# Kernel tuning notes

Measured on AMD Instinct MI355X. Metric: run time of the kernel, lower is better.

## Reference

```python
import jax, jax.numpy as jnp
import numpy as np

# NF4 codebook (bitsandbytes NormalFloat4 quantiles)
NF4_TABLE = jnp.array([
    -1.0, -0.6961928009986877, -0.5250730514526367, -0.39491748809814453,
    -0.28444138169288635, -0.18477343022823334, -0.09105003625154495, 0.0,
    0.07958029955625534, 0.16093020141124725, 0.24611230194568634,
    0.33791524171829224, 0.44070982933044434, 0.5626170039176941,
    0.7229568362236023, 1.0], dtype=jnp.float32)

BLOCK = 64  # bitsandbytes default quantization blocksize


def setup_inputs() -> dict:
    key = jax.random.key(0)
    ks = jax.random.split(key, 6)
    in_f, out_f, rank, n_tok = 4096, 4096, 16, 8192
    x = jax.random.normal(ks[0], (n_tok, in_f), dtype=jnp.float32)
    q_codes = jax.random.randint(ks[1], (out_f, in_f), 0, 16, dtype=jnp.int32)
    absmax = jax.random.uniform(ks[2], (out_f, in_f // BLOCK), dtype=jnp.float32) * 0.1 + 1e-3
    bias = jax.random.normal(ks[3], (out_f,), dtype=jnp.float32) * 0.02
    # kaiming-uniform-ish init for lora_down; lora_up nonzero for a meaningful test
    lora_down_w = jax.random.normal(ks[4], (rank, in_f), dtype=jnp.float32) * (1.0 / np.sqrt(in_f))
    lora_up_w = jax.random.normal(ks[5], (out_f, rank), dtype=jnp.float32) * 0.02
    alpha = jnp.array(16.0, dtype=jnp.float32)
    return {"x": x, "absmax": absmax, "bias": bias, "lora_down_w": lora_down_w,
            "lora_up_w": lora_up_w, "alpha": alpha, "q_codes": q_codes}


def reference(x, absmax, bias, lora_down_w, lora_up_w, alpha, q_codes):
    rank = lora_down_w.shape[0]
    # dequantize NF4 base weight: code lookup * per-block absmax scale
    w = NF4_TABLE[q_codes] * jnp.repeat(absmax, BLOCK, axis=1)  # [out, in]
    base = x @ w.T + bias                                       # [n_tok, out]
    # LoRA path: down [rank,in], up [out,rank], scaled by alpha/rank
    lora = (x @ lora_down_w.T) @ lora_up_w.T                    # [n_tok, out]
    return base + lora * (alpha / rank)
```

## Files before the change

kernel.cpp:

```cpp
#include <hip/hip_runtime.h>

#define IN_F 4096
#define OUT_F 4096
#define RANK 16
#define NTOK 8192
#define KP 4160
#define BK 64
#define NT (KP / BK)
#define BM 256
#define BN 256

typedef __bf16 bf16x8 __attribute__((ext_vector_type(8)));
typedef float f32x4 __attribute__((ext_vector_type(4)));

__device__ __forceinline__ unsigned short f2bf(float f) {
  unsigned int u = __float_as_uint(f);
  u += 0x7fffu + ((u >> 16) & 1u);
  return (unsigned short)(u >> 16);
}

__device__ __forceinline__ void async_ld16(const void* g, void* l) {
  __builtin_amdgcn_global_load_lds(
      (const __attribute__((address_space(1))) unsigned int*)g,
      (__attribute__((address_space(3))) unsigned int*)l, 16, 0, 0);
}

__device__ const float NF4_TAB[16] = {
    -1.0f, -0.6961928009986877f, -0.5250730514526367f, -0.39491748809814453f,
    -0.28444138169288635f, -0.18477343022823334f, -0.09105003625154495f, 0.0f,
    0.07958029955625534f, 0.16093020141124725f, 0.24611230194568634f,
    0.33791524171829224f, 0.44070982933044434f, 0.5626170039176941f,
    0.7229568362236023f, 1.0f};

__global__ __launch_bounds__(256) void k_prep_a(
    const float* __restrict__ x, const float* __restrict__ ldw,
    unsigned short* __restrict__ Ap) {
  const int tid = threadIdx.x;
  const int lane = tid & 63;
  const int w = tid >> 6;
  const int m0 = blockIdx.x * 4;

  float acc[4][4];
#pragma unroll
  for (int i = 0; i < 4; ++i)
#pragma unroll
    for (int rl = 0; rl < 4; ++rl) acc[i][rl] = 0.f;

  for (int c = 0; c < 16; ++c) {
    const int k0 = (c * 64 + lane) * 4;
    float4 xv[4];
#pragma unroll
    for (int i = 0; i < 4; ++i) {
      xv[i] = *(const float4*)&x[(size_t)(m0 + i) * IN_F + k0];
      if (w == 0) {
        ushort4 s;
        s.x = f2bf(xv[i].x); s.y = f2bf(xv[i].y);
        s.z = f2bf(xv[i].z); s.w = f2bf(xv[i].w);
        *(ushort4*)&Ap[(size_t)(m0 + i) * KP + k0] = s;
      }
    }
#pragma unroll
    for (int rl = 0; rl < 4; ++rl) {
      float4 lv = *(const float4*)&ldw[(size_t)(w * 4 + rl) * IN_F + k0];
#pragma unroll
      for (int i = 0; i < 4; ++i)
        acc[i][rl] += xv[i].x * lv.x + xv[i].y * lv.y + xv[i].z * lv.z +
                      xv[i].w * lv.w;
    }
  }
#pragma unroll
  for (int i = 0; i < 4; ++i)
#pragma unroll
    for (int rl = 0; rl < 4; ++rl) {
      float v = acc[i][rl];
#pragma unroll
      for (int m = 1; m < 64; m <<= 1) v += __shfl_xor(v, m, 64);
      acc[i][rl] = v;
    }
  __shared__ float red[4][16];
  if (lane == 0) {
#pragma unroll
    for (int i = 0; i < 4; ++i)
#pragma unroll
      for (int rl = 0; rl < 4; ++rl) red[i][w * 4 + rl] = acc[i][rl];
  }
  __syncthreads();
  if (tid < 64) {
    Ap[(size_t)(m0 + (tid >> 4)) * KP + IN_F + (tid & 15)] =
        f2bf(red[tid >> 4][tid & 15]);
  } else {
    const int t2 = tid - 64;
    if (t2 < 192)
      Ap[(size_t)(m0 + t2 / 48) * KP + IN_F + 16 + (t2 % 48)] = 0;
  }
}

__global__ __launch_bounds__(256) void k_prep_b(
    const int* __restrict__ q, const float* __restrict__ amax,
    const float* __restrict__ luw, const float* __restrict__ alpha,
    unsigned short* __restrict__ Bp) {
  __shared__ float tab[16];
  const int tid = threadIdx.x;
  const int n = blockIdx.x;
  if (tid < 16) tab[tid] = NF4_TAB[tid];
  __syncthreads();
#pragma unroll
  for (int c = 0; c < 4; ++c) {
    const int k0 = (tid + 256 * c) * 4;
    int4 qv = *(const int4*)&q[(size_t)n * IN_F + k0];
    float am = amax[n * (IN_F / 64) + (k0 >> 6)];
    ushort4 s;
    s.x = f2bf(tab[qv.x] * am);
    s.y = f2bf(tab[qv.y] * am);
    s.z = f2bf(tab[qv.z] * am);
    s.w = f2bf(tab[qv.w] * am);
    *(ushort4*)&Bp[(size_t)n * KP + k0] = s;
  }
  if (tid < RANK) {
    float sc = alpha[0] * (1.0f / RANK);
    Bp[(size_t)n * KP + IN_F + tid] = f2bf(luw[n * RANK + tid] * sc);
  } else if (tid < 64) {
    Bp[(size_t)n * KP + IN_F + tid] = 0;
  }
}

__global__ __launch_bounds__(512, 1) void k_gemm(
    const unsigned short* __restrict__ Ap, const unsigned short* __restrict__ Bp,
    const float* __restrict__ bias, float* __restrict__ out) {
  __shared__ unsigned short lds[65536];
  const int tid = threadIdx.x;
  const int lane = tid & 63;
  const int w = tid >> 6;
  const int wr = w >> 2;
  const int wc = w & 3;

  const int nwg = gridDim.x * gridDim.y;
  const int flat = blockIdx.y * gridDim.x + blockIdx.x;
  const int cpx = nwg >> 3;
  const int swz = (flat & 7) * cpx + (flat >> 3);
  const int m0 = (swz / (OUT_F / BN)) * BM;
  const int n0 = (swz % (OUT_F / BN)) * BN;

  const int srow = lane >> 3;
  const int scol = (((lane & 7) ^ srow) << 3);
  const unsigned short* gA = Ap + (size_t)(m0 + (w << 4) + srow) * KP + scol;
  const unsigned short* gB = Bp + (size_t)(n0 + (w << 4) + srow) * KP + scol;
  unsigned short* const ldsw = lds + (w << 10);

  const int rdoff = ((lane & 15) << 6) + (((lane >> 4) ^ (lane & 7)) << 3);

#define STAGE2(tt, ht, cond)                                                   \
  if (cond) {                                                                  \
    const unsigned short* s_ =                                                 \
        ((ht) < 2 ? gA + (size_t)((ht) << 7) * KP                              \
                  : gB + (size_t)(((ht)-2) << 7) * KP) + (size_t)(tt)*BK;      \
    unsigned short* d_ = ldsw + ((((tt)&1) << 15) + ((ht) << 13));             \
    async_ld16(s_, d_);                                                        \
    async_ld16(s_ + (size_t)8 * KP, d_ + 512);                                 \
  }

#define LDA(bsel, mh, f, kc)                                                   \
  (*(const bf16x8*)&lds[((bsel) << 15) + (wr << 13) +                          \
                        (((mh)*64 + (f)*16) << 6) + (((kc) << 5) ^ rdoff)])
#define LDB(bsel, nh, g, kc)                                                   \
  (*(const bf16x8*)&lds[((bsel) << 15) + ((2 + (wc >> 1)) << 13) +             \
                        ((((wc & 1) * 64) + (nh)*32 + (g)*16) << 6) +          \
                        (((kc) << 5) ^ rdoff)])

#define MFMA(a, b, c) __builtin_amdgcn_mfma_f32_16x16x32_bf16((a), (b), (c), 0, 0, 0)

  STAGE2(0, 0, true) STAGE2(0, 1, true) STAGE2(0, 2, true) STAGE2(0, 3, true)
  STAGE2(1, 0, true) STAGE2(1, 1, true)
  asm volatile("s_waitcnt vmcnt(4)" ::: "memory");
  __builtin_amdgcn_s_barrier();

  f32x4 acc[8][4] = {};
  bf16x8 a0[4][2], a1[4][2], bq[2][2];

#pragma unroll 2
  for (int t = 0; t < NT; ++t) {
    const int bsel = t & 1;
#pragma unroll
    for (int f = 0; f < 4; ++f) {
      a0[f][0] = LDA(bsel, 0, f, 0);
      a0[f][1] = LDA(bsel, 0, f, 1);
    }
#pragma unroll
    for (int g = 0; g < 2; ++g) {
      bq[g][0] = LDB(bsel, 0, g, 0);
      bq[g][1] = LDB(bsel, 0, g, 1);
    }
    STAGE2(t + 1, 2, t + 1 < NT)
    __builtin_amdgcn_s_barrier();
    asm volatile("s_waitcnt lgkmcnt(0)" ::: "memory");
    __builtin_amdgcn_sched_barrier(0);
    __builtin_amdgcn_s_setprio(1);
#pragma unroll
    for (int f = 0; f < 4; ++f)
#pragma unroll
      for (int g = 0; g < 2; ++g) {
        acc[f][g] = MFMA(a0[f][0], bq[g][0], acc[f][g]);
        acc[f][g] = MFMA(a0[f][1], bq[g][1], acc[f][g]);
      }
    __builtin_amdgcn_s_setprio(0);
    __builtin_amdgcn_s_barrier();
#pragma unroll
    for (int f = 0; f < 4; ++f) {
      a1[f][0] = LDA(bsel, 1, f, 0);
      a1[f][1] = LDA(bsel, 1, f, 1);
    }
    STAGE2(t + 1, 3, t + 1 < NT)
    __builtin_amdgcn_s_barrier();
    asm volatile("s_waitcnt lgkmcnt(0)" ::: "memory");
    __builtin_amdgcn_sched_barrier(0);
    __builtin_amdgcn_s_setprio(1);
#pragma unroll
    for (int f = 0; f < 4; ++f)
#pragma unroll
      for (int g = 0; g < 2; ++g) {
        acc[4 + f][g] = MFMA(a1[f][0], bq[g][0], acc[4 + f][g]);
        acc[4 + f][g] = MFMA(a1[f][1], bq[g][1], acc[4 + f][g]);
      }
    __builtin_amdgcn_s_setprio(0);
    __builtin_amdgcn_s_barrier();
#pragma unroll
    for (int g = 0; g < 2; ++g) {
      bq[g][0] = LDB(bsel, 1, g, 0);
      bq[g][1] = LDB(bsel, 1, g, 1);
    }
    STAGE2(t + 2, 0, t + 2 < NT)
    __builtin_amdgcn_s_barrier();
    asm volatile("s_waitcnt lgkmcnt(0)" ::: "memory");
    __builtin_amdgcn_sched_barrier(0);
    __builtin_amdgcn_s_setprio(1);
#pragma unroll
    for (int f = 0; f < 4; ++f)
#pragma unroll
      for (int g = 0; g < 2; ++g) {
        acc[4 + f][2 + g] = MFMA(a1[f][0], bq[g][0], acc[4 + f][2 + g]);
        acc[4 + f][2 + g] = MFMA(a1[f][1], bq[g][1], acc[4 + f][2 + g]);
      }
    __builtin_amdgcn_s_setprio(0);
    __builtin_amdgcn_s_barrier();
    STAGE2(t + 2, 1, t + 2 < NT)
    __builtin_amdgcn_s_barrier();
    asm volatile("s_waitcnt lgkmcnt(0)" ::: "memory");
    __builtin_amdgcn_sched_barrier(0);
    __builtin_amdgcn_s_setprio(1);
#pragma unroll
    for (int f = 0; f < 4; ++f)
#pragma unroll
      for (int g = 0; g < 2; ++g) {
        acc[f][2 + g] = MFMA(a0[f][0], bq[g][0], acc[f][2 + g]);
        acc[f][2 + g] = MFMA(a0[f][1], bq[g][1], acc[f][2 + g]);
      }
    __builtin_amdgcn_s_setprio(0);
    if (t < NT - 2) {
      asm volatile("s_waitcnt vmcnt(4)" ::: "memory");
    } else if (t == NT - 2) {
      asm volatile("s_waitcnt vmcnt(0)" ::: "memory");
    }
    __builtin_amdgcn_s_barrier();
    __builtin_amdgcn_sched_barrier(0);
  }

  const int colL = lane & 15;
  const int rowG = lane >> 4;
#pragma unroll
  for (int nj = 0; nj < 4; ++nj) {
    const int n = n0 + wc * 64 + nj * 16 + colL;
    const float bv = bias[n];
#pragma unroll
    for (int mi = 0; mi < 8; ++mi) {
      const int mb = m0 + wr * 128 + mi * 16 + rowG * 4;
#pragma unroll
      for (int e = 0; e < 4; ++e)
        out[(size_t)(mb + e) * OUT_F + n] = acc[mi][nj][e] + bv;
    }
  }
#undef STAGE2
#undef LDA
#undef LDB
#undef MFMA
}

extern "C" void kernel_launch(void* const* d_in, const int* in_sizes, int n_in,
                              void* d_out, int out_size, void* d_ws, size_t ws_size,
                              hipStream_t stream) {
  (void)in_sizes; (void)n_in; (void)out_size; (void)ws_size;
  const float* x     = (const float*)d_in[0];
  const float* amax  = (const float*)d_in[1];
  const float* bias  = (const float*)d_in[2];
  const float* ldw   = (const float*)d_in[3];
  const float* luw   = (const float*)d_in[4];
  const float* alpha = (const float*)d_in[5];
  const int*   q     = (const int*)d_in[6];
  float* out = (float*)d_out;

  unsigned short* Ap = (unsigned short*)d_ws;
  unsigned short* Bp = Ap + (size_t)NTOK * KP;

  k_prep_a<<<NTOK / 4, 256, 0, stream>>>(x, ldw, Ap);
  k_prep_b<<<OUT_F, 256, 0, stream>>>(q, amax, luw, alpha, Bp);
  k_gemm<<<dim3(OUT_F / BN, NTOK / BM), 512, 0, stream>>>(Ap, Bp, bias, out);
}
```

Baseline: 351.3 us.

## Switch main GEMM to 32x32x16 bf16 MFMA with reworked LDS fragment loads

Replaces the 16x16x32 MFMA tiling with 32x32x16 MFMA instructions, restructuring the per-wave fragment loads from swizzled LDS and the accumulator layout (f32x16 tiles), plus a matching epilogue. The larger MFMA cuts the number of LDS fragment reads per flop and the instruction count. It also drops one lgkmcnt wait before the last MFMA group, since that group reuses already-loaded registers. Separately, the prep kernel now spreads the bf16 conversion stores across four waves instead of one.

```diff
diff --git a/kernel.cpp b/kernel.cpp
--- a/kernel.cpp
+++ b/kernel.cpp
@@ -12,6 +12,7 @@
 
 typedef __bf16 bf16x8 __attribute__((ext_vector_type(8)));
 typedef float f32x4 __attribute__((ext_vector_type(4)));
+typedef float f32x16 __attribute__((ext_vector_type(16)));
 
 __device__ __forceinline__ unsigned short f2bf(float f) {
   unsigned int u = __float_as_uint(f);
@@ -52,7 +53,7 @@
 #pragma unroll
     for (int i = 0; i < 4; ++i) {
       xv[i] = *(const float4*)&x[(size_t)(m0 + i) * IN_F + k0];
-      if (w == 0) {
+      if (w == i) {
         ushort4 s;
         s.x = f2bf(xv[i].x); s.y = f2bf(xv[i].y);
         s.z = f2bf(xv[i].z); s.w = f2bf(xv[i].w);
@@ -147,7 +148,9 @@
   const unsigned short* gB = Bp + (size_t)(n0 + (w << 4) + srow) * KP + scol;
   unsigned short* const ldsw = lds + (w << 10);
 
-  const int rdoff = ((lane & 15) << 6) + (((lane >> 4) ^ (lane & 7)) << 3);
+  const int rowA = (lane & 31) << 6;
+  const int hi = lane >> 5;
+  const int sw = lane & 7;
 
 #define STAGE2(tt, ht, cond)                                                   \
   if (cond) {                                                                  \
@@ -159,36 +162,32 @@
     async_ld16(s_ + (size_t)8 * KP, d_ + 512);                                 \
   }
 
-#define LDA(bsel, mh, f, kc)                                                   \
-  (*(const bf16x8*)&lds[((bsel) << 15) + (wr << 13) +                          \
-                        (((mh)*64 + (f)*16) << 6) + (((kc) << 5) ^ rdoff)])
-#define LDB(bsel, nh, g, kc)                                                   \
+#define LDA32(bsel, tm, s)                                                     \
+  (*(const bf16x8*)&lds[((bsel) << 15) + (wr << 13) + ((tm) << 11) + rowA +    \
+                        (((((s) << 1) | hi) ^ sw) << 3)])
+#define LDB32(bsel, tn, s)                                                     \
   (*(const bf16x8*)&lds[((bsel) << 15) + ((2 + (wc >> 1)) << 13) +             \
-                        ((((wc & 1) * 64) + (nh)*32 + (g)*16) << 6) +          \
-                        (((kc) << 5) ^ rdoff)])
-
-#define MFMA(a, b, c) __builtin_amdgcn_mfma_f32_16x16x32_bf16((a), (b), (c), 0, 0, 0)
+                        ((wc & 1) << 12) + ((tn) << 11) + rowA +               \
+                        (((((s) << 1) | hi) ^ sw) << 3)])
+
+#define MFMA32(a, b, c) __builtin_amdgcn_mfma_f32_32x32x16_bf16((a), (b), (c), 0, 0, 0)
 
   STAGE2(0, 0, true) STAGE2(0, 1, true) STAGE2(0, 2, true) STAGE2(0, 3, true)
   STAGE2(1, 0, true) STAGE2(1, 1, true)
   asm volatile("s_waitcnt vmcnt(4)" ::: "memory");
   __builtin_amdgcn_s_barrier();
 
-  f32x4 acc[8][4] = {};
-  bf16x8 a0[4][2], a1[4][2], bq[2][2];
+  f32x16 acc[4][2] = {};
+  bf16x8 a01[2][4], a23[2][4], bq[4];
 
 #pragma unroll 2
   for (int t = 0; t < NT; ++t) {
     const int bsel = t & 1;
 #pragma unroll
-    for (int f = 0; f < 4; ++f) {
-      a0[f][0] = LDA(bsel, 0, f, 0);
-      a0[f][1] = LDA(bsel, 0, f, 1);
-    }
-#pragma unroll
-    for (int g = 0; g < 2; ++g) {
-      bq[g][0] = LDB(bsel, 0, g, 0);
-      bq[g][1] = LDB(bsel, 0, g, 1);
+    for (int s = 0; s < 4; ++s) {
+      a01[0][s] = LDA32(bsel, 0, s);
+      a01[1][s] = LDA32(bsel, 1, s);
+      bq[s] = LDB32(bsel, 0, s);
     }
     STAGE2(t + 1, 2, t + 1 < NT)
     __builtin_amdgcn_s_barrier();
@@ -196,18 +195,16 @@
     __builtin_amdgcn_sched_barrier(0);
     __builtin_amdgcn_s_setprio(1);
 #pragma unroll
-    for (int f = 0; f < 4; ++f)
-#pragma unroll
-      for (int g = 0; g < 2; ++g) {
-        acc[f][g] = MFMA(a0[f][0], bq[g][0], acc[f][g]);
-        acc[f][g] = MFMA(a0[f][1], bq[g][1], acc[f][g]);
-      }
-    __builtin_amdgcn_s_setprio(0);
-    __builtin_amdgcn_s_barrier();
-#pragma unroll
-    for (int f = 0; f < 4; ++f) {
-      a1[f][0] = LDA(bsel, 1, f, 0);
-      a1[f][1] = LDA(bsel, 1, f, 1);
+    for (int s = 0; s < 4; ++s) {
+      acc[0][0] = MFMA32(a01[0][s], bq[s], acc[0][0]);
+      acc[1][0] = MFMA32(a01[1][s], bq[s], acc[1][0]);
+    }
+    __builtin_amdgcn_s_setprio(0);
+    __builtin_amdgcn_s_barrier();
+#pragma unroll
+    for (int s = 0; s < 4; ++s) {
+      a23[0][s] = LDA32(bsel, 2, s);
+      a23[1][s] = LDA32(bsel, 3, s);
     }
     STAGE2(t + 1, 3, t + 1 < NT)
     __builtin_amdgcn_s_barrier();
@@ -215,45 +212,35 @@
     __builtin_amdgcn_sched_barrier(0);
     __builtin_amdgcn_s_setprio(1);
 #pragma unroll
-    for (int f = 0; f < 4; ++f)
-#pragma unroll
-      for (int g = 0; g < 2; ++g) {
-        acc[4 + f][g] = MFMA(a1[f][0], bq[g][0], acc[4 + f][g]);
-        acc[4 + f][g] = MFMA(a1[f][1], bq[g][1], acc[4 + f][g]);
-      }
-    __builtin_amdgcn_s_setprio(0);
-    __builtin_amdgcn_s_barrier();
-#pragma unroll
-    for (int g = 0; g < 2; ++g) {
-      bq[g][0] = LDB(bsel, 1, g, 0);
-      bq[g][1] = LDB(bsel, 1, g, 1);
-    }
+    for (int s = 0; s < 4; ++s) {
+      acc[2][0] = MFMA32(a23[0][s], bq[s], acc[2][0]);
+      acc[3][0] = MFMA32(a23[1][s], bq[s], acc[3][0]);
+    }
+    __builtin_amdgcn_s_setprio(0);
+    __builtin_amdgcn_s_barrier();
+#pragma unroll
+    for (int s = 0; s < 4; ++s) bq[s] = LDB32(bsel, 1, s);
     STAGE2(t + 2, 0, t + 2 < NT)
     __builtin_amdgcn_s_barrier();
     asm volatile("s_waitcnt lgkmcnt(0)" ::: "memory");
     __builtin_amdgcn_sched_barrier(0);
     __builtin_amdgcn_s_setprio(1);
 #pragma unroll
-    for (int f = 0; f < 4; ++f)
-#pragma unroll
-      for (int g = 0; g < 2; ++g) {
-        acc[4 + f][2 + g] = MFMA(a1[f][0], bq[g][0], acc[4 + f][2 + g]);
-        acc[4 + f][2 + g] = MFMA(a1[f][1], bq[g][1], acc[4 + f][2 + g]);
-      }
+    for (int s = 0; s < 4; ++s) {
+      acc[2][1] = MFMA32(a23[0][s], bq[s], acc[2][1]);
+      acc[3][1] = MFMA32(a23[1][s], bq[s], acc[3][1]);
+    }
     __builtin_amdgcn_s_setprio(0);
     __builtin_amdgcn_s_barrier();
     STAGE2(t + 2, 1, t + 2 < NT)
     __builtin_amdgcn_s_barrier();
-    asm volatile("s_waitcnt lgkmcnt(0)" ::: "memory");
-    __builtin_amdgcn_sched_barrier(0);
-    __builtin_amdgcn_s_setprio(1);
-#pragma unroll
-    for (int f = 0; f < 4; ++f)
-#pragma unroll
-      for (int g = 0; g < 2; ++g) {
-        acc[f][2 + g] = MFMA(a0[f][0], bq[g][0], acc[f][2 + g]);
-        acc[f][2 + g] = MFMA(a0[f][1], bq[g][1], acc[f][2 + g]);
-      }
+    __builtin_amdgcn_sched_barrier(0);
+    __builtin_amdgcn_s_setprio(1);
+#pragma unroll
+    for (int s = 0; s < 4; ++s) {
+      acc[0][1] = MFMA32(a01[0][s], bq[s], acc[0][1]);
+      acc[1][1] = MFMA32(a01[1][s], bq[s], acc[1][1]);
+    }
     __builtin_amdgcn_s_setprio(0);
     if (t < NT - 2) {
       asm volatile("s_waitcnt vmcnt(4)" ::: "memory");
@@ -264,24 +251,26 @@
     __builtin_amdgcn_sched_barrier(0);
   }
 
-  const int colL = lane & 15;
-  const int rowG = lane >> 4;
-#pragma unroll
-  for (int nj = 0; nj < 4; ++nj) {
-    const int n = n0 + wc * 64 + nj * 16 + colL;
+  const int colL = lane & 31;
+  const int rowH = hi << 2;
+#pragma unroll
+  for (int tn = 0; tn < 2; ++tn) {
+    const int n = n0 + wc * 64 + tn * 32 + colL;
     const float bv = bias[n];
 #pragma unroll
-    for (int mi = 0; mi < 8; ++mi) {
-      const int mb = m0 + wr * 128 + mi * 16 + rowG * 4;
-#pragma unroll
-      for (int e = 0; e < 4; ++e)
-        out[(size_t)(mb + e) * OUT_F + n] = acc[mi][nj][e] + bv;
+    for (int tm = 0; tm < 4; ++tm) {
+      const int mb = m0 + wr * 128 + tm * 32 + rowH;
+#pragma unroll
+      for (int r = 0; r < 16; ++r) {
+        const int row = mb + (r & 3) + ((r >> 2) << 3);
+        out[(size_t)row * OUT_F + n] = acc[tm][tn][r] + bv;
+      }
     }
   }
 #undef STAGE2
-#undef LDA
-#undef LDB
-#undef MFMA
+#undef LDA32
+#undef LDB32
+#undef MFMA32
 }
 
 extern "C" void kernel_launch(void* const* d_in, const int* in_sizes, int n_in,
```

Result: slower. 371.8 us (+5.8%).
